# Optimization experiments

Hardware: AMD Instinct MI355X
Metric: run time of the kernel (lower is better)

## Reference

```python
import jax, jax.numpy as jnp
import numpy as np

CHUNK = 64  # rows of `a` processed per step to bound the [chunk, N, d] abs-diff intermediate
TAIL_K = 4          # selection_tail_size
FAR_K = 64          # far_sample_count
PUSH_K = 4          # pushing_sample_size
HUBER_DELTA = 1.0   # torch.nn.HuberLoss default


def cdist_l1(a, b):
    # a: [M, d], b: [N, d] -> [M, N] Manhattan distances, computed in row chunks
    M, d = a.shape
    def f(a_chunk):  # [CHUNK, d] -> [CHUNK, N]
        return jnp.abs(a_chunk[:, None, :] - b[None, :, :]).sum(-1)
    return jax.lax.map(f, a.reshape(-1, CHUNK, d)).reshape(M, b.shape[0])


def smallest_k_mean(dists, k):
    # mean of the k smallest entries along last dim
    neg_vals, _ = jax.lax.top_k(-dists, k)
    return (-neg_vals).mean(-1)


def huber(x):
    # HuberLoss(pred=x, target=0), delta=1
    ax = jnp.abs(x)
    return jnp.where(ax < HUBER_DELTA, 0.5 * x * x, HUBER_DELTA * (ax - 0.5 * HUBER_DELTA))


def setup_inputs() -> dict:
    key = jax.random.key(0)
    k1, k2 = jax.random.split(key)
    space_samples = jax.random.normal(k1, (2048, 256), dtype=jnp.float32)
    latents = jax.random.normal(k2, (8192, 256), dtype=jnp.float32)
    return {"space_samples": space_samples, "latents": latents}


def reference(space_samples, latents):
    # space_samples: [M, d] drawn from latent_sampler; latents: [N, d]
    space_dists = cdist_l1(space_samples, latents)            # [M, N]
    tail_dists = smallest_k_mean(space_dists, TAIL_K)          # [M]
    far_inds = jax.lax.top_k(tail_dists, FAR_K)[1]             # [FAR_K]
    far_samples = space_samples[far_inds]                      # [FAR_K, d]
    empty_dists = cdist_l1(far_samples, latents)               # [FAR_K, N]
    close_dists = smallest_k_mean(empty_dists, PUSH_K)         # [FAR_K]
    return huber(close_dists).mean()
```

## Files before the change

### kernel.cpp

```cpp
#include <hip/hip_runtime.h>
#include <hip/hip_bf16.h>


static constexpr int M = 2048;
static constexpr int N = 8192;
static constexpr int KQ = 64;
static constexpr int BKQ = 16;
static constexpr int ROWS_PER_BLK = 128;
static constexpr int COLS_PER_BLK = 128;
static constexpr int NCHUNK = N / COLS_PER_BLK;
static constexpr int SLD_RED = 68;

static constexpr float QS  = 21.0f;
static constexpr float QB  = 126.0f;
static constexpr float INV_QS = 1.0f / 21.0f;

__device__ __forceinline__ float med3f(float a, float b, float c) {
    return __builtin_amdgcn_fmed3f(a, b, c);
}

__device__ __forceinline__ void ins4(float d, float& s0, float& s1, float& s2, float& s3) {
    float n0 = fminf(s0, d);
    float n1 = med3f(s0, s1, d);
    float n2 = med3f(s1, s2, d);
    float n3 = med3f(s2, s3, d);
    s0 = n0; s1 = n1; s2 = n2; s3 = n3;
}

__device__ __forceinline__ unsigned int sad8(unsigned int a, unsigned int b, unsigned int c) {
#if __has_builtin(__builtin_amdgcn_sad_u8)
    return __builtin_amdgcn_sad_u8(a, b, c);
#else
    unsigned int d;
    asm("v_sad_u8 %0, %1, %2, %3" : "=v"(d) : "v"(a), "v"(b), "v"(c));
    return d;
#endif
}

__device__ __forceinline__ unsigned int quant4(const float4 v) {
    const float y0 = fminf(fmaxf(fmaf(v.x, QS, QB), 0.0f), 255.0f);
    const float y1 = fminf(fmaxf(fmaf(v.y, QS, QB), 0.0f), 255.0f);
    const float y2 = fminf(fmaxf(fmaf(v.z, QS, QB), 0.0f), 255.0f);
    const float y3 = fminf(fmaxf(fmaf(v.w, QS, QB), 0.0f), 255.0f);
    const unsigned int b0 = (unsigned int)(int)rintf(y0);
    const unsigned int b1 = (unsigned int)(int)rintf(y1);
    const unsigned int b2 = (unsigned int)(int)rintf(y2);
    const unsigned int b3 = (unsigned int)(int)rintf(y3);
    return b0 | (b1 << 8) | (b2 << 16) | (b3 << 24);
}

__global__ __launch_bounds__(256)
void convert_kernel(const float* __restrict__ A, const float* __restrict__ B,
                    unsigned int* __restrict__ At, unsigned int* __restrict__ Bt) {
    const int idx = blockIdx.x * 256 + threadIdx.x;
    if (idx < N * 32) {
        const int g = idx >> 13;
        const int n = idx & (N - 1);
        const float4 v0 = *(const float4*)&B[n * 256 + 8 * g];
        const float4 v1 = *(const float4*)&B[n * 256 + 8 * g + 4];
        Bt[(2 * g) * N + n]     = quant4(v0);
        Bt[(2 * g + 1) * N + n] = quant4(v1);
    } else {
        const int idx2 = idx - N * 32;
        const int g = idx2 >> 11;
        const int n = idx2 & (M - 1);
        const float4 v0 = *(const float4*)&A[n * 256 + 8 * g];
        const float4 v1 = *(const float4*)&A[n * 256 + 8 * g + 4];
        At[(2 * g) * M + n]     = quant4(v0);
        At[(2 * g + 1) * M + n] = quant4(v1);
    }
}

__global__ __launch_bounds__(256, 4)
void dist4_kernel(const unsigned int* __restrict__ At, const unsigned int* __restrict__ Bt,
                  float4* __restrict__ ws_dist) {
    __shared__ __align__(16) char smem[34816];
    unsigned int* tiles = (unsigned int*)smem;
    const int tid = threadIdx.x;
    const int tx = tid & 15;
    const int ty = tid >> 4;
    const int bx = blockIdx.x;
    const int by = blockIdx.y;
    const int rowBase = by * ROWS_PER_BLK;
    const int colBase = bx * COLS_PER_BLK;

    const int sKq = tid >> 5;
    const int sC  = (tid & 31) * 4;

    unsigned int acc[8][8];
#pragma unroll
    for (int i = 0; i < 8; ++i)
#pragma unroll
        for (int j = 0; j < 8; ++j) acc[i][j] = 0u;

    uint4 pa0, pa1, pb0, pb1;
    pa0 = *(const uint4*)&At[(sKq) * M + rowBase + sC];
    pa1 = *(const uint4*)&At[(sKq + 8) * M + rowBase + sC];
    pb0 = *(const uint4*)&Bt[(sKq) * N + colBase + sC];
    pb1 = *(const uint4*)&Bt[(sKq + 8) * N + colBase + sC];
    {
        unsigned int* As = tiles;
        unsigned int* Bs = tiles + 2048;
        *(uint4*)&As[sKq * 128 + sC] = pa0;
        *(uint4*)&As[(sKq + 8) * 128 + sC] = pa1;
        *(uint4*)&Bs[sKq * 128 + sC] = pb0;
        *(uint4*)&Bs[(sKq + 8) * 128 + sC] = pb1;
    }

    for (int t0 = 0; t0 < KQ / BKQ; ++t0) {
        __syncthreads();
        if (t0 + 1 < KQ / BKQ) {
            const int kb = (t0 + 1) * BKQ;
            pa0 = *(const uint4*)&At[(kb + sKq) * M + rowBase + sC];
            pa1 = *(const uint4*)&At[(kb + sKq + 8) * M + rowBase + sC];
            pb0 = *(const uint4*)&Bt[(kb + sKq) * N + colBase + sC];
            pb1 = *(const uint4*)&Bt[(kb + sKq + 8) * N + colBase + sC];
        }

        const unsigned int* As = tiles + (t0 & 1) * 4096;
        const unsigned int* Bs = As + 2048;
#pragma unroll 4
        for (int kq = 0; kq < BKQ; ++kq) {
            const uint4 aw0 = *(const uint4*)&As[kq * 128 + 8 * ty];
            const uint4 aw1 = *(const uint4*)&As[kq * 128 + 8 * ty + 4];
            const uint4 bw0 = *(const uint4*)&Bs[kq * 128 + 4 * tx];
            const uint4 bw1 = *(const uint4*)&Bs[kq * 128 + 64 + 4 * tx];
            const unsigned int a[8] = {aw0.x, aw0.y, aw0.z, aw0.w, aw1.x, aw1.y, aw1.z, aw1.w};
            const unsigned int b[8] = {bw0.x, bw0.y, bw0.z, bw0.w, bw1.x, bw1.y, bw1.z, bw1.w};
#pragma unroll
            for (int i = 0; i < 8; ++i) {
#pragma unroll
                for (int j = 0; j < 8; ++j) {
                    acc[i][j] = sad8(a[i], b[j], acc[i][j]);
                }
            }
        }

        if (t0 + 1 < KQ / BKQ) {
            __syncthreads();
            unsigned int* Asw = tiles + ((t0 + 1) & 1) * 4096;
            unsigned int* Bsw = Asw + 2048;
            *(uint4*)&Asw[sKq * 128 + sC] = pa0;
            *(uint4*)&Asw[(sKq + 8) * 128 + sC] = pa1;
            *(uint4*)&Bsw[sKq * 128 + sC] = pb0;
            *(uint4*)&Bsw[(sKq + 8) * 128 + sC] = pb1;
        }
    }

    float s[8][4];
#pragma unroll
    for (int i = 0; i < 8; ++i) {
        float s0 = 1e30f, s1 = 1e30f, s2 = 1e30f, s3 = 1e30f;
#pragma unroll
        for (int j = 0; j < 8; ++j) {
            const float d = (float)acc[i][j] * INV_QS;
            ins4(d, s0, s1, s2, s3);
        }
        s[i][0] = s0; s[i][1] = s1; s[i][2] = s2; s[i][3] = s3;
    }

    __syncthreads();
    float (*red)[SLD_RED] = (float (*)[SLD_RED])smem;
#pragma unroll
    for (int i = 0; i < 8; ++i) {
        *(float4*)&red[8 * ty + i][4 * tx] = make_float4(s[i][0], s[i][1], s[i][2], s[i][3]);
    }
    __syncthreads();

    if (tid < ROWS_PER_BLK) {
        float s0 = 1e30f, s1 = 1e30f, s2 = 1e30f, s3 = 1e30f;
#pragma unroll
        for (int c = 0; c < 16; ++c) {
            const float4 v = *(const float4*)&red[tid][4 * c];
            ins4(v.x, s0, s1, s2, s3);
            ins4(v.y, s0, s1, s2, s3);
            ins4(v.z, s0, s1, s2, s3);
            ins4(v.w, s0, s1, s2, s3);
        }
        ws_dist[bx * M + rowBase + tid] = make_float4(s0, s1, s2, s3);
    }
}

__global__ __launch_bounds__(256)
void tail_kernel(const float4* __restrict__ ws_dist, float* __restrict__ tail) {
    const int r = blockIdx.x * 256 + threadIdx.x;
    float s0 = 1e30f, s1 = 1e30f, s2 = 1e30f, s3 = 1e30f;
#pragma unroll
    for (int c = 0; c < NCHUNK; ++c) {
        const float4 v = ws_dist[c * M + r];
        ins4(v.x, s0, s1, s2, s3);
        ins4(v.y, s0, s1, s2, s3);
        ins4(v.z, s0, s1, s2, s3);
        ins4(v.w, s0, s1, s2, s3);
    }
    tail[r] = (s0 + s1 + s2 + s3) * 0.25f;
}

__global__ __launch_bounds__(1024)
void top64_kernel(const float* __restrict__ tail, float* __restrict__ out) {
    __shared__ float sh[M];
    const int tid = threadIdx.x;
    sh[tid] = tail[tid];
    sh[tid + 1024] = tail[tid + 1024];
    __syncthreads();

    for (int k = 2; k <= M; k <<= 1) {
        for (int j = k >> 1; j > 0; j >>= 1) {
#pragma unroll
            for (int half = 0; half < 2; ++half) {
                const int i = tid + half * 1024;
                const int ixj = i ^ j;
                if (ixj > i) {
                    const float a = sh[i];
                    const float b = sh[ixj];
                    const bool desc = ((i & k) == 0);
                    const bool sw = desc ? (a < b) : (a > b);
                    if (sw) { sh[i] = b; sh[ixj] = a; }
                }
            }
            __syncthreads();
        }
    }

    if (tid < 64) {
        const float x = sh[tid];
        const float ax = __builtin_fabsf(x);
        float h = (ax < 1.0f) ? (0.5f * x * x) : (ax - 0.5f);
#pragma unroll
        for (int off = 32; off > 0; off >>= 1) {
            h += __shfl_down(h, off, 64);
        }
        if (tid == 0) out[0] = h * (1.0f / 64.0f);
    }
}

extern "C" void kernel_launch(void* const* d_in, const int* in_sizes, int n_in,
                              void* d_out, int out_size, void* d_ws, size_t ws_size,
                              hipStream_t stream) {
    const float* A = (const float*)d_in[0];
    const float* B = (const float*)d_in[1];
    float* out = (float*)d_out;

    unsigned int* Bt = (unsigned int*)d_ws;
    unsigned int* At = (unsigned int*)((char*)d_ws + (size_t)KQ * N * 4);
    float4* ws_dist = (float4*)((char*)d_ws + (size_t)KQ * N * 4 + (size_t)KQ * M * 4);
    float* tail = (float*)((char*)ws_dist + (size_t)NCHUNK * M * sizeof(float4));

    convert_kernel<<<dim3((N * 32 + M * 32) / 256), 256, 0, stream>>>(A, B, At, Bt);
    dist4_kernel<<<dim3(NCHUNK, M / ROWS_PER_BLK), 256, 0, stream>>>(At, Bt, ws_dist);
    tail_kernel<<<dim3(M / 256), 256, 0, stream>>>(ws_dist, tail);
    top64_kernel<<<1, 1024, 0, stream>>>(tail, out);
}
```

Baseline: 132.3 us.

## Replace sort-based top-64 with radix select and shuffle-reduce per-row minima

```diff
diff --git a/kernel.cpp b/kernel.cpp
--- a/kernel.cpp
+++ b/kernel.cpp
@@ -9,7 +9,6 @@
 static constexpr int ROWS_PER_BLK = 128;
 static constexpr int COLS_PER_BLK = 128;
 static constexpr int NCHUNK = N / COLS_PER_BLK;
-static constexpr int SLD_RED = 68;
 
 static constexpr float QS  = 21.0f;
 static constexpr float QB  = 126.0f;
@@ -47,6 +46,11 @@
     const unsigned int b2 = (unsigned int)(int)rintf(y2);
     const unsigned int b3 = (unsigned int)(int)rintf(y3);
     return b0 | (b1 << 8) | (b2 << 16) | (b3 << 24);
+}
+
+__device__ __forceinline__ float huber_pos(float x) {
+    const float ax = __builtin_fabsf(x);
+    return (ax < 1.0f) ? (0.5f * x * x) : (ax - 0.5f);
 }
 
 __global__ __launch_bounds__(256)
@@ -71,11 +75,10 @@
     }
 }
 
-__global__ __launch_bounds__(256, 4)
+__global__ __launch_bounds__(256, 5)
 void dist4_kernel(const unsigned int* __restrict__ At, const unsigned int* __restrict__ Bt,
                   float4* __restrict__ ws_dist) {
-    __shared__ __align__(16) char smem[34816];
-    unsigned int* tiles = (unsigned int*)smem;
+    __shared__ __align__(16) unsigned int tiles[8192];
     const int tid = threadIdx.x;
     const int tx = tid & 15;
     const int ty = tid >> 4;
@@ -159,78 +162,142 @@
         s[i][0] = s0; s[i][1] = s1; s[i][2] = s2; s[i][3] = s3;
     }
 
-    __syncthreads();
-    float (*red)[SLD_RED] = (float (*)[SLD_RED])smem;
-#pragma unroll
-    for (int i = 0; i < 8; ++i) {
-        *(float4*)&red[8 * ty + i][4 * tx] = make_float4(s[i][0], s[i][1], s[i][2], s[i][3]);
-    }
-    __syncthreads();
-
-    if (tid < ROWS_PER_BLK) {
-        float s0 = 1e30f, s1 = 1e30f, s2 = 1e30f, s3 = 1e30f;
-#pragma unroll
-        for (int c = 0; c < 16; ++c) {
-            const float4 v = *(const float4*)&red[tid][4 * c];
-            ins4(v.x, s0, s1, s2, s3);
-            ins4(v.y, s0, s1, s2, s3);
-            ins4(v.z, s0, s1, s2, s3);
-            ins4(v.w, s0, s1, s2, s3);
-        }
-        ws_dist[bx * M + rowBase + tid] = make_float4(s0, s1, s2, s3);
+#pragma unroll
+    for (int lvl = 1; lvl <= 8; lvl <<= 1) {
+#pragma unroll
+        for (int i = 0; i < 8; ++i) {
+            const float o0 = __shfl_xor(s[i][0], lvl, 64);
+            const float o1 = __shfl_xor(s[i][1], lvl, 64);
+            const float o2 = __shfl_xor(s[i][2], lvl, 64);
+            const float o3 = __shfl_xor(s[i][3], lvl, 64);
+            ins4(o0, s[i][0], s[i][1], s[i][2], s[i][3]);
+            ins4(o1, s[i][0], s[i][1], s[i][2], s[i][3]);
+            ins4(o2, s[i][0], s[i][1], s[i][2], s[i][3]);
+            ins4(o3, s[i][0], s[i][1], s[i][2], s[i][3]);
+        }
+    }
+
+    if (tx == 0) {
+#pragma unroll
+        for (int i = 0; i < 8; ++i) {
+            ws_dist[bx * M + rowBase + 8 * ty + i] =
+                make_float4(s[i][0], s[i][1], s[i][2], s[i][3]);
+        }
     }
 }
 
 __global__ __launch_bounds__(256)
 void tail_kernel(const float4* __restrict__ ws_dist, float* __restrict__ tail) {
-    const int r = blockIdx.x * 256 + threadIdx.x;
+    const int gtid = blockIdx.x * 256 + threadIdx.x;
+    const int row = gtid >> 2;
+    const int q = gtid & 3;
     float s0 = 1e30f, s1 = 1e30f, s2 = 1e30f, s3 = 1e30f;
 #pragma unroll
-    for (int c = 0; c < NCHUNK; ++c) {
-        const float4 v = ws_dist[c * M + r];
+    for (int c = 0; c < 16; ++c) {
+        const float4 v = ws_dist[(q * 16 + c) * M + row];
         ins4(v.x, s0, s1, s2, s3);
         ins4(v.y, s0, s1, s2, s3);
         ins4(v.z, s0, s1, s2, s3);
         ins4(v.w, s0, s1, s2, s3);
     }
-    tail[r] = (s0 + s1 + s2 + s3) * 0.25f;
+#pragma unroll
+    for (int lvl = 1; lvl <= 2; lvl <<= 1) {
+        const float o0 = __shfl_xor(s0, lvl, 64);
+        const float o1 = __shfl_xor(s1, lvl, 64);
+        const float o2 = __shfl_xor(s2, lvl, 64);
+        const float o3 = __shfl_xor(s3, lvl, 64);
+        ins4(o0, s0, s1, s2, s3);
+        ins4(o1, s0, s1, s2, s3);
+        ins4(o2, s0, s1, s2, s3);
+        ins4(o3, s0, s1, s2, s3);
+    }
+    if (q == 0) tail[row] = (s0 + s1 + s2 + s3) * 0.25f;
 }
 
 __global__ __launch_bounds__(1024)
 void top64_kernel(const float* __restrict__ tail, float* __restrict__ out) {
-    __shared__ float sh[M];
+    __shared__ unsigned int hist[8][256];
+    __shared__ unsigned int ctrl[2];
+    __shared__ float wsum[16];
+    __shared__ unsigned int wcnt[16];
     const int tid = threadIdx.x;
-    sh[tid] = tail[tid];
-    sh[tid + 1024] = tail[tid + 1024];
-    __syncthreads();
-
-    for (int k = 2; k <= M; k <<= 1) {
-        for (int j = k >> 1; j > 0; j >>= 1) {
-#pragma unroll
-            for (int half = 0; half < 2; ++half) {
-                const int i = tid + half * 1024;
-                const int ixj = i ^ j;
-                if (ixj > i) {
-                    const float a = sh[i];
-                    const float b = sh[ixj];
-                    const bool desc = ((i & k) == 0);
-                    const bool sw = desc ? (a < b) : (a > b);
-                    if (sw) { sh[i] = b; sh[ixj] = a; }
+    const int wid = tid >> 6;
+    const int lane = tid & 63;
+
+    const unsigned int k0 = __float_as_uint(tail[tid]);
+    const unsigned int k1 = __float_as_uint(tail[tid + 1024]);
+
+    if (tid == 0) { ctrl[0] = 0u; ctrl[1] = 64u; }
+
+    for (int p = 0; p < 4; ++p) {
+        const int shift = 24 - 8 * p;
+        ((unsigned int*)hist)[tid] = 0u;
+        ((unsigned int*)hist)[tid + 1024] = 0u;
+        __syncthreads();
+        const unsigned int prefix = ctrl[0];
+        const unsigned int t = ctrl[1];
+        bool c0 = true, c1 = true;
+        if (p > 0) {
+            const int sh8 = shift + 8;
+            c0 = ((k0 >> sh8) == (prefix >> sh8));
+            c1 = ((k1 >> sh8) == (prefix >> sh8));
+        }
+        if (c0) atomicAdd(&hist[wid & 7][(k0 >> shift) & 255], 1u);
+        if (c1) atomicAdd(&hist[wid & 7][(k1 >> shift) & 255], 1u);
+        __syncthreads();
+        if (tid < 256) {
+            unsigned int h = 0;
+#pragma unroll
+            for (int r = 0; r < 8; ++r) h += hist[r][tid];
+            hist[0][tid] = h;
+        }
+        __syncthreads();
+        if (wid == 0) {
+            const unsigned int s4 = hist[0][4 * lane] + hist[0][4 * lane + 1] +
+                                    hist[0][4 * lane + 2] + hist[0][4 * lane + 3];
+            unsigned int suf = s4;
+#pragma unroll
+            for (int off = 1; off < 64; off <<= 1) {
+                const unsigned int v = __shfl_down(suf, off, 64);
+                if (lane + off < 64) suf += v;
+            }
+            const unsigned long long mask = __ballot(suf >= t);
+            const int lstar = 63 - __clzll(mask);
+            if (lane == lstar) {
+                unsigned int c = suf - s4;
+                for (int d = 4 * lstar + 3; d >= 4 * lstar; --d) {
+                    const unsigned int cd = hist[0][d];
+                    c += cd;
+                    if (c >= t) {
+                        ctrl[0] = prefix | ((unsigned int)d << shift);
+                        ctrl[1] = t - (c - cd);
+                        break;
+                    }
                 }
             }
-            __syncthreads();
-        }
-    }
-
-    if (tid < 64) {
-        const float x = sh[tid];
-        const float ax = __builtin_fabsf(x);
-        float h = (ax < 1.0f) ? (0.5f * x * x) : (ax - 0.5f);
-#pragma unroll
-        for (int off = 32; off > 0; off >>= 1) {
-            h += __shfl_down(h, off, 64);
-        }
-        if (tid == 0) out[0] = h * (1.0f / 64.0f);
+        }
+        __syncthreads();
+    }
+
+    const unsigned int T = ctrl[0];
+    float sum = 0.0f;
+    unsigned int cnt = 0;
+    if (k0 > T) { ++cnt; sum += huber_pos(__uint_as_float(k0)); }
+    if (k1 > T) { ++cnt; sum += huber_pos(__uint_as_float(k1)); }
+#pragma unroll
+    for (int off = 32; off > 0; off >>= 1) {
+        sum += __shfl_down(sum, off, 64);
+        cnt += __shfl_down(cnt, off, 64);
+    }
+    if (lane == 0) { wsum[wid] = sum; wcnt[wid] = cnt; }
+    __syncthreads();
+    if (tid == 0) {
+        float S = 0.0f;
+        unsigned int C = 0;
+#pragma unroll
+        for (int w = 0; w < 16; ++w) { S += wsum[w]; C += wcnt[w]; }
+        const float hT = huber_pos(__uint_as_float(T));
+        out[0] = (S + (float)(64u - C) * hT) * (1.0f / 64.0f);
     }
 }
 
@@ -248,6 +315,6 @@
 
     convert_kernel<<<dim3((N * 32 + M * 32) / 256), 256, 0, stream>>>(A, B, At, Bt);
     dist4_kernel<<<dim3(NCHUNK, M / ROWS_PER_BLK), 256, 0, stream>>>(At, Bt, ws_dist);
-    tail_kernel<<<dim3(M / 256), 256, 0, stream>>>(ws_dist, tail);
+    tail_kernel<<<dim3(M * 4 / 256), 256, 0, stream>>>(ws_dist, tail);
     top64_kernel<<<1, 1024, 0, stream>>>(tail, out);
 }
```

Measured after the change: 125.3 us. -5.3%, faster.
